# Kernel tuning notes

Measured on AMD Instinct MI355X. Metric: run time of the kernel, lower is better.

The kernel has to match this reference:

```python
import jax, jax.numpy as jnp
import numpy as np

POOL = (2, 2)
STRIDES = (2, 2)


def _maxpool2d(x):
    # NHWC max pooling, VALID padding (matches K.pool2d(..., pool_mode='max'))
    return jax.lax.reduce_window(
        x, -jnp.inf, jax.lax.max,
        window_dimensions=(1, POOL[0], POOL[1], 1),
        window_strides=(1, STRIDES[0], STRIDES[1], 1),
        padding='VALID')


def setup_inputs() -> dict:
    key = jax.random.key(0)
    ks = jax.random.split(key, 8)
    B, H, W, C = 2, 64, 64, 128
    n_out = 32
    n_pool = (H // POOL[0]) * (W // POOL[1]) * C  # 131072
    y = jax.random.normal(ks[0], (B, H, W, C), jnp.float32)
    x_0 = jax.random.normal(ks[1], (B, 16), jnp.float32)
    mid = jax.random.normal(ks[2], (B, H, W, C), jnp.float32)
    rad = jax.random.uniform(ks[3], (B, H, W, C), jnp.float32)
    u_c = mid + rad  # valid interval bounds: l_c <= u_c
    l_c = mid - rad
    w_out_u = jax.random.normal(ks[4], (B, 1, n_pool, n_out), jnp.float32)
    b_out_u = jax.random.normal(ks[5], (B, 1, n_out), jnp.float32)
    w_out_l = jax.random.normal(ks[6], (B, 1, n_pool, n_out), jnp.float32)
    b_out_l = jax.random.normal(ks[7], (B, 1, n_out), jnp.float32)
    return {"y": y, "x_0": x_0, "u_c": u_c, "l_c": l_c,
            "w_out_u": w_out_u, "b_out_u": b_out_u,
            "w_out_l": w_out_l, "b_out_l": b_out_l}


def reference(y, x_0, u_c, l_c, w_out_u, b_out_u, w_out_l, b_out_l):
    # BackwardMaxPooling2D._pooling_function_fast, mode=F_IBP
    B = y.shape[0]
    # b_u_, b_l_: (B, 1, n_pool, 1) constant post-pool bounds
    b_u = _maxpool2d(u_c).reshape(B, 1, -1, 1)
    b_l = _maxpool2d(l_c).reshape(B, 1, -1, 1)
    n_in = int(np.prod(y.shape[1:]))
    n_out = w_out_u.shape[-1]
    # w_out_u_ = concat([0 * flatten(y)] * n_out) -> identically zero weights
    w_zero = jnp.broadcast_to(0.0 * y.reshape(B, 1, n_in, 1), (B, 1, n_in, n_out))
    # fold backward weights into constant biases using interval bounds
    b_out_u_ = (jnp.sum(jnp.maximum(w_out_u, 0.0) * b_u, axis=2)
                + jnp.sum(jnp.minimum(w_out_u, 0.0) * b_l, axis=2)
                + b_out_u)
    b_out_l_ = (jnp.sum(jnp.maximum(w_out_l, 0.0) * b_l, axis=2)
                + jnp.sum(jnp.minimum(w_out_l, 0.0) * b_u, axis=2)
                + b_out_l)
    return (w_zero, b_out_u_, w_zero, b_out_l_)
```

## Files before the change

### kernel.cpp

```cpp
#include <hip/hip_runtime.h>

#define BATCH 2
#define HH 64
#define WW 64
#define CC 128
#define OHH 32
#define OWW 32
#define NPOOL (OHH * OWW * CC)
#define NOUT 32
#define NIN (HH * WW * CC)
#define WZERO ((size_t)BATCH * NIN * NOUT)

#define OFF_BU (WZERO)
#define OFF_BL (2 * WZERO + (size_t)BATCH * NOUT)

#define CHUNKS 128
#define PPC (NPOOL / CHUNKS)
#define RBLOCKS (BATCH * CHUNKS)

#define ZBLOCKS 2048
#define ZQUADS ((2 * WZERO) / 4)
#define ZPB (ZQUADS / ZBLOCKS)
#define R1Q (WZERO / 4)
#define GAPQ (((size_t)BATCH * NOUT) / 4)

__global__ void __launch_bounds__(256) fused_kernel(
        const float4* __restrict__ u_c,
        const float4* __restrict__ l_c,
        const float4* __restrict__ wu,
        const float4* __restrict__ wl,
        float4* __restrict__ partial,
        float* __restrict__ out) {
    const int blk = blockIdx.x;
    const int t = threadIdx.x;

    if (blk >= RBLOCKS) {
        const size_t z0 = (size_t)(blk - RBLOCKS) * ZPB;
        const float4 zero = make_float4(0.f, 0.f, 0.f, 0.f);
        float4* o4 = (float4*)out;
        #pragma unroll
        for (int i = 0; i < ZPB / 256; ++i) {
            size_t q = z0 + (size_t)i * 256 + t;
            size_t addr = (q < R1Q) ? q : q + GAPQ;
            o4[addr] = zero;
        }
        return;
    }

    const int b = blk / CHUNKS;
    const int chunk = blk % CHUNKS;

    __shared__ float4 pu4[256];
    __shared__ float4 pl4[256];

    {
        const int sp = t >> 5;
        const int c4 = t & 31;
        const int s = chunk * 8 + sp;
        const int oh = s >> 5;
        const int ow = s & 31;
        const int base = ((b * HH + 2 * oh) * WW + 2 * ow) * (CC / 4) + c4;
        const int cs = CC / 4;
        const int rs = WW * (CC / 4);
        {
            float4 a0 = u_c[base];
            float4 a1 = u_c[base + cs];
            float4 a2 = u_c[base + rs];
            float4 a3 = u_c[base + rs + cs];
            float4 m;
            m.x = fmaxf(fmaxf(a0.x, a1.x), fmaxf(a2.x, a3.x));
            m.y = fmaxf(fmaxf(a0.y, a1.y), fmaxf(a2.y, a3.y));
            m.z = fmaxf(fmaxf(a0.z, a1.z), fmaxf(a2.z, a3.z));
            m.w = fmaxf(fmaxf(a0.w, a1.w), fmaxf(a2.w, a3.w));
            pu4[t] = m;
        }
        {
            float4 a0 = l_c[base];
            float4 a1 = l_c[base + cs];
            float4 a2 = l_c[base + rs];
            float4 a3 = l_c[base + rs + cs];
            float4 m;
            m.x = fmaxf(fmaxf(a0.x, a1.x), fmaxf(a2.x, a3.x));
            m.y = fmaxf(fmaxf(a0.y, a1.y), fmaxf(a2.y, a3.y));
            m.z = fmaxf(fmaxf(a0.z, a1.z), fmaxf(a2.z, a3.z));
            m.w = fmaxf(fmaxf(a0.w, a1.w), fmaxf(a2.w, a3.w));
            pl4[t] = m;
        }
    }
    __syncthreads();

    const float* puf = (const float*)pu4;
    const float* plf = (const float*)pl4;

    const int og = t & 7;
    const int pln = t >> 3;

    float4 au = make_float4(0.f, 0.f, 0.f, 0.f);
    float4 al = make_float4(0.f, 0.f, 0.f, 0.f);

    const size_t wbase =
        ((size_t)b * NPOOL + (size_t)chunk * PPC) * (NOUT / 4) + og;

    #pragma unroll 8
    for (int k = 0; k < PPC / 32; ++k) {
        const int lp = pln + 32 * k;
        const float vbu = puf[lp];
        const float vbl = plf[lp];
        const float4 u4 = wu[wbase + (size_t)lp * (NOUT / 4)];
        const float4 l4 = wl[wbase + (size_t)lp * (NOUT / 4)];
        au.x += fmaxf(u4.x, 0.f) * vbu + fminf(u4.x, 0.f) * vbl;
        au.y += fmaxf(u4.y, 0.f) * vbu + fminf(u4.y, 0.f) * vbl;
        au.z += fmaxf(u4.z, 0.f) * vbu + fminf(u4.z, 0.f) * vbl;
        au.w += fmaxf(u4.w, 0.f) * vbu + fminf(u4.w, 0.f) * vbl;
        al.x += fmaxf(l4.x, 0.f) * vbl + fminf(l4.x, 0.f) * vbu;
        al.y += fmaxf(l4.y, 0.f) * vbl + fminf(l4.y, 0.f) * vbu;
        al.z += fmaxf(l4.z, 0.f) * vbl + fminf(l4.z, 0.f) * vbu;
        al.w += fmaxf(l4.w, 0.f) * vbl + fminf(l4.w, 0.f) * vbu;
    }

    __syncthreads();
    pu4[t] = au;
    pl4[t] = al;
    __syncthreads();
    for (int s = 128; s >= 8; s >>= 1) {
        if (t < s) {
            float4 xu = pu4[t + s];
            pu4[t].x += xu.x; pu4[t].y += xu.y;
            pu4[t].z += xu.z; pu4[t].w += xu.w;
            float4 xl = pl4[t + s];
            pl4[t].x += xl.x; pl4[t].y += xl.y;
            pl4[t].z += xl.z; pl4[t].w += xl.w;
        }
        __syncthreads();
    }

    if (t < 8) {
        partial[(size_t)blk * 16 + t] = pu4[t];
        partial[(size_t)blk * 16 + 8 + t] = pl4[t];
    }
}

__global__ void finish_kernel(const float* __restrict__ partial,
                              const float* __restrict__ b_out_u,
                              const float* __restrict__ b_out_l,
                              float* __restrict__ out) {
    const int t = threadIdx.x;
    const int b = t >> 6;
    const int uo = (t >> 5) & 1;
    const int o = t & 31;
    float s = 0.f;
    for (int chunk = 0; chunk < CHUNKS; ++chunk) {
        s += partial[((size_t)(b * CHUNKS + chunk)) * 64 + uo * 32 + o];
    }
    if (uo == 0) {
        out[OFF_BU + (size_t)b * NOUT + o] = s + b_out_u[b * NOUT + o];
    } else {
        out[OFF_BL + (size_t)b * NOUT + o] = s + b_out_l[b * NOUT + o];
    }
}

extern "C" void kernel_launch(void* const* d_in, const int* in_sizes, int n_in,
                              void* d_out, int out_size, void* d_ws, size_t ws_size,
                              hipStream_t stream) {
    const float* u_c     = (const float*)d_in[2];
    const float* l_c     = (const float*)d_in[3];
    const float* w_out_u = (const float*)d_in[4];
    const float* b_out_u = (const float*)d_in[5];
    const float* w_out_l = (const float*)d_in[6];
    const float* b_out_l = (const float*)d_in[7];
    float* out = (float*)d_out;

    float4* ws_partial = (float4*)d_ws;

    fused_kernel<<<RBLOCKS + ZBLOCKS, 256, 0, stream>>>(
        (const float4*)u_c, (const float4*)l_c,
        (const float4*)w_out_u, (const float4*)w_out_l,
        ws_partial, out);

    finish_kernel<<<1, 128, 0, stream>>>(
        (const float*)ws_partial, b_out_u, b_out_l, out);
}
```

Before: 338.6 us.

## Split zero-fill into its own kernel and quadruple reduction chunk count

The fused kernel is split in two: a reduction kernel and a separate grid-stride kernel that zero-fills the weight outputs. Reduction chunks go from 128 to 512 per batch, so there are more, smaller blocks with a fully unrolled inner loop and a smaller shared pooling buffer. The aim is more parallelism for the weight-streaming reduction and a simpler zero-fill store loop. In exchange, the zero-fill and the reduction now run one after the other instead of overlapping in one launch, which adds a kernel launch and may lose concurrency on the store-bound part.

```diff
diff --git a/kernel.cpp b/kernel.cpp
--- a/kernel.cpp
+++ b/kernel.cpp
@@ -14,49 +14,47 @@
 #define OFF_BU (WZERO)
 #define OFF_BL (2 * WZERO + (size_t)BATCH * NOUT)
 
-#define CHUNKS 128
+#define CHUNKS 512
 #define PPC (NPOOL / CHUNKS)
+#define SPC (PPC / CC)
 #define RBLOCKS (BATCH * CHUNKS)
 
 #define ZBLOCKS 2048
-#define ZQUADS ((2 * WZERO) / 4)
-#define ZPB (ZQUADS / ZBLOCKS)
 #define R1Q (WZERO / 4)
+#define TOTQ (2 * R1Q)
 #define GAPQ (((size_t)BATCH * NOUT) / 4)
 
-__global__ void __launch_bounds__(256) fused_kernel(
+__global__ void __launch_bounds__(256) zero_kernel(float4* __restrict__ out4) {
+    const float4 z = make_float4(0.f, 0.f, 0.f, 0.f);
+    size_t i = (size_t)blockIdx.x * 256 + threadIdx.x;
+    const size_t stride = (size_t)ZBLOCKS * 256;
+    #pragma unroll 8
+    for (; i < TOTQ; i += stride) {
+        size_t addr = (i < R1Q) ? i : i + GAPQ;
+        out4[addr] = z;
+    }
+}
+
+__global__ void __launch_bounds__(256) reduce_kernel(
         const float4* __restrict__ u_c,
         const float4* __restrict__ l_c,
         const float4* __restrict__ wu,
         const float4* __restrict__ wl,
-        float4* __restrict__ partial,
-        float* __restrict__ out) {
+        float4* __restrict__ partial) {
     const int blk = blockIdx.x;
     const int t = threadIdx.x;
-
-    if (blk >= RBLOCKS) {
-        const size_t z0 = (size_t)(blk - RBLOCKS) * ZPB;
-        const float4 zero = make_float4(0.f, 0.f, 0.f, 0.f);
-        float4* o4 = (float4*)out;
-        #pragma unroll
-        for (int i = 0; i < ZPB / 256; ++i) {
-            size_t q = z0 + (size_t)i * 256 + t;
-            size_t addr = (q < R1Q) ? q : q + GAPQ;
-            o4[addr] = zero;
-        }
-        return;
-    }
-
     const int b = blk / CHUNKS;
     const int chunk = blk % CHUNKS;
 
-    __shared__ float4 pu4[256];
-    __shared__ float4 pl4[256];
+    __shared__ float4 pu4[PPC / 4];
+    __shared__ float4 pl4[PPC / 4];
+    __shared__ float4 su[256];
+    __shared__ float4 sl[256];
 
-    {
+    if (t < (PPC / 4)) {
         const int sp = t >> 5;
         const int c4 = t & 31;
-        const int s = chunk * 8 + sp;
+        const int s = chunk * SPC + sp;
         const int oh = s >> 5;
         const int ow = s & 31;
         const int base = ((b * HH + 2 * oh) * WW + 2 * ow) * (CC / 4) + c4;
@@ -101,7 +99,7 @@
     const size_t wbase =
         ((size_t)b * NPOOL + (size_t)chunk * PPC) * (NOUT / 4) + og;
 
-    #pragma unroll 8
+    #pragma unroll
     for (int k = 0; k < PPC / 32; ++k) {
         const int lp = pln + 32 * k;
         const float vbu = puf[lp];
@@ -118,25 +116,24 @@
         al.w += fmaxf(l4.w, 0.f) * vbl + fminf(l4.w, 0.f) * vbu;
     }
 
-    __syncthreads();
-    pu4[t] = au;
-    pl4[t] = al;
+    su[t] = au;
+    sl[t] = al;
     __syncthreads();
     for (int s = 128; s >= 8; s >>= 1) {
         if (t < s) {
-            float4 xu = pu4[t + s];
-            pu4[t].x += xu.x; pu4[t].y += xu.y;
-            pu4[t].z += xu.z; pu4[t].w += xu.w;
-            float4 xl = pl4[t + s];
-            pl4[t].x += xl.x; pl4[t].y += xl.y;
-            pl4[t].z += xl.z; pl4[t].w += xl.w;
+            float4 xu = su[t + s];
+            su[t].x += xu.x; su[t].y += xu.y;
+            su[t].z += xu.z; su[t].w += xu.w;
+            float4 xl = sl[t + s];
+            sl[t].x += xl.x; sl[t].y += xl.y;
+            sl[t].z += xl.z; sl[t].w += xl.w;
         }
         __syncthreads();
     }
 
     if (t < 8) {
-        partial[(size_t)blk * 16 + t] = pu4[t];
-        partial[(size_t)blk * 16 + 8 + t] = pl4[t];
+        partial[(size_t)blk * 16 + t] = su[t];
+        partial[(size_t)blk * 16 + 8 + t] = sl[t];
     }
 }
 
@@ -172,10 +169,12 @@
 
     float4* ws_partial = (float4*)d_ws;
 
-    fused_kernel<<<RBLOCKS + ZBLOCKS, 256, 0, stream>>>(
+    reduce_kernel<<<RBLOCKS, 256, 0, stream>>>(
         (const float4*)u_c, (const float4*)l_c,
         (const float4*)w_out_u, (const float4*)w_out_l,
-        ws_partial, out);
+        ws_partial);
+
+    zero_kernel<<<ZBLOCKS, 256, 0, stream>>>((float4*)out);
 
     finish_kernel<<<1, 128, 0, stream>>>(
         (const float*)ws_partial, b_out_u, b_out_l, out);
```

After: 362.0 us. 6.9% more time.
